# Performance work log

Measured on AMD Instinct MI355X. Metric: run time of the kernel, lower is better.

## Reference

```python
import jax, jax.numpy as jnp
import numpy as np

N_NODES, N_EDGES, D_IN, D_OUT = 50000, 800000, 64, 64
N_REL, N_TIME = 500, 1000


def setup_inputs() -> dict:
    key = jax.random.key(0)
    ks = jax.random.split(key, 14)
    xavier = lambda k, shape: jax.random.normal(k, shape, jnp.float32) * np.sqrt(2.0 / (shape[0] + shape[1])) * np.sqrt(2.0)
    return {
        "x": jax.random.normal(ks[0], (N_NODES, D_IN), jnp.float32),
        "rel_repr": jax.random.normal(ks[1], (N_REL, D_IN), jnp.float32),
        "time_emds": jax.random.normal(ks[2], (N_TIME, D_IN), jnp.float32),
        "src": jax.random.randint(ks[3], (N_EDGES,), 0, N_NODES),
        "dst": jax.random.randint(ks[4], (N_EDGES,), 0, N_NODES),
        "etype": jax.random.randint(ks[5], (N_EDGES,), 0, N_REL),
        "etime": jax.random.randint(ks[6], (N_EDGES,), 0, N_TIME),
        "trans_w": xavier(ks[7], (D_IN, D_OUT)),
        "loop_w": xavier(ks[8], (D_IN, D_OUT)),
        "w_rel": xavier(ks[9], (D_IN, D_OUT)),
        "attn_h": xavier(ks[10], (D_IN, 1)),
        "attn_t": xavier(ks[11], (D_IN, 1)),
        "attn_r": xavier(ks[12], (D_IN, 1)),
        "attn_ts": xavier(ks[13], (D_IN, 1)),
    }


def reference(x, rel_repr, time_emds, src, dst, etype, etime,
              trans_w, loop_w, w_rel, attn_h, attn_t, attn_r, attn_ts):
    n = x.shape[0]
    # per-node / per-rel / per-time scalar attention projections
    h_att = (x @ attn_h)[:, 0]          # [N]
    t_att = (x @ attn_t)[:, 0]          # [N]
    r_att = (rel_repr @ attn_r)[:, 0]   # [R]
    ts_att = (time_emds @ attn_ts)[:, 0]  # [T]
    # edge attention logits + edge_softmax grouped by destination node
    e = jax.nn.leaky_relu(h_att[src] - t_att[dst] + r_att[etype] + ts_att[etime], 0.1)  # [E]
    m = jax.ops.segment_max(e, dst, num_segments=n)
    ex = jnp.exp(e - m[dst])
    den = jax.ops.segment_sum(ex, dst, num_segments=n)
    att = (ex / den[dst])[:, None]      # [E,1]
    # message: (head + time) * (rel + time) -> trans_w -> weighted scatter-sum to dst
    time_emd = time_emds[etime]         # [E,D]
    edge_data = (x[src] + time_emd) * (rel_repr[etype] + time_emd)
    msg = (edge_data @ trans_w) * att   # [E,D_out]
    h = jax.ops.segment_sum(msg, dst, num_segments=n)
    x_out = h + x @ loop_w
    rel_out = rel_repr @ w_rel
    return (x_out, rel_out)
```

## Files before the change

kernel.cpp:

```cpp
#include <hip/hip_runtime.h>
#include <hip/hip_bf16.h>

#define N_NODES 50000
#define N_EDGES 800000
#define D 64
#define N_REL 500
#define N_TIME 1000
#define SLOTS 64
#define NODE_BLOCKS ((N_NODES + 63) / 64)
#define REL_BLOCKS  ((N_REL + 63) / 64)

#define CB 64
#define NCB ((N_NODES + CB - 1) / CB)
#define FR 64
#define NFB ((N_NODES + FR - 1) / FR)
#define SCAP 2048
#define BINCAP 8
#define BTILE 4096
#define LSLOT 48

__device__ __forceinline__ float bf2f(unsigned short u) {
    union { unsigned int i; float f; } v;
    v.i = ((unsigned int)u) << 16;
    return v.f;
}

__global__ void proj_kernel(const float* __restrict__ x,
                            const float* __restrict__ rel,
                            const float* __restrict__ tim,
                            const float* __restrict__ ah,
                            const float* __restrict__ at,
                            const float* __restrict__ ar,
                            const float* __restrict__ ats,
                            float* __restrict__ h_att, float* __restrict__ t_att,
                            float* __restrict__ r_att, float* __restrict__ ts_att,
                            unsigned short* __restrict__ x_bf,
                            int* __restrict__ cursor) {
    int gid = blockIdx.x * blockDim.x + threadIdx.x;
    if (gid < NCB) cursor[gid] = 0;
    int wave = gid >> 6;
    int lane = threadIdx.x & 63;
    const int total = N_NODES + N_REL + N_TIME;
    if (wave >= total) return;
    if (wave < N_NODES) {
        float xv = x[wave * D + lane];
        __hip_bfloat16 b = __float2bfloat16(xv);
        x_bf[wave * D + lane] = *(unsigned short*)&b;
        float s1 = xv * ah[lane];
        float s2 = xv * at[lane];
        for (int off = 32; off; off >>= 1) {
            s1 += __shfl_down(s1, off);
            s2 += __shfl_down(s2, off);
        }
        if (lane == 0) { h_att[wave] = s1; t_att[wave] = s2; }
    } else if (wave < N_NODES + N_REL) {
        int r = wave - N_NODES;
        float v = rel[r * D + lane] * ar[lane];
        for (int off = 32; off; off >>= 1) v += __shfl_down(v, off);
        if (lane == 0) r_att[r] = v;
    } else {
        int t = wave - N_NODES - N_REL;
        float v = tim[t * D + lane] * ats[lane];
        for (int off = 32; off; off >>= 1) v += __shfl_down(v, off);
        if (lane == 0) ts_att[t] = v;
    }
}

__global__ __launch_bounds__(512)
void bin_kernel(const int* __restrict__ src, const int* __restrict__ dst,
                const int* __restrict__ etype, const int* __restrict__ etime,
                const float* __restrict__ h_att, const float* __restrict__ t_att,
                const float* __restrict__ r_att, const float* __restrict__ ts_att,
                int* __restrict__ cursor, int4* __restrict__ stage) {
    __shared__ int4 bins[NCB][BINCAP];
    __shared__ int bcnt[NCB];
    int t = threadIdx.x;
    for (int k = t; k < NCB; k += 512) bcnt[k] = 0;
    __syncthreads();

    int e0 = blockIdx.x * BTILE;
    for (int j = 0; j < 8; j++) {
        int e = e0 + j * 512 + t;
        if (e < N_EDGES) {
            int s = src[e], d = dst[e], r = etype[e], tt = etime[e];
            float lg = h_att[s] - t_att[d] + r_att[r] + ts_att[tt];
            float lr = lg > 0.f ? lg : 0.1f * lg;
            float ex = __expf(lr);
            unsigned exb = __float_as_uint(ex);
            int4 rec;
            rec.x = (int)((exb & ~7u) | (unsigned)(s & 7));
            rec.y = (int)(((unsigned)(s >> 3) << 19) | ((unsigned)r << 10) | (unsigned)tt);
            rec.z = d;
            rec.w = 0;
            int k = d >> 6;
            int pos = atomicAdd(&bcnt[k], 1);
            if (pos < BINCAP) {
                bins[k][pos] = rec;
            } else {
                int g = atomicAdd(&cursor[k], 1);
                if (g < SCAP) stage[(size_t)k * SCAP + g] = rec;
            }
        }
    }
    __syncthreads();
    for (int k = t; k < NCB; k += 512) {
        int c = bcnt[k];
        if (c > BINCAP) c = BINCAP;
        if (c > 0) {
            int base = atomicAdd(&cursor[k], c);
            for (int i = 0; i < c; i++) {
                int g = base + i;
                if (g < SCAP) stage[(size_t)k * SCAP + g] = bins[k][i];
            }
        }
    }
}

__global__ __launch_bounds__(512)
void node_fused_kernel(const unsigned short* __restrict__ x_bf,
                       const float* __restrict__ rel,
                       const float* __restrict__ tim,
                       const int* __restrict__ cursor,
                       const int4* __restrict__ stage,
                       float* __restrict__ agg) {
    __shared__ int2 lslot[FR * LSLOT];
    __shared__ int lcnt[FR];
    int tid = threadIdx.x;
    int base = blockIdx.x * FR;
    int pb = blockIdx.x;

    for (int i = tid; i < FR; i += 512) lcnt[i] = 0;
    __syncthreads();

    int n = cursor[pb];
    if (n > SCAP) n = SCAP;
    for (int i = tid; i < n; i += 512) {
        int4 rec = stage[(size_t)pb * SCAP + i];
        int ln = rec.z - base;
        if ((unsigned)ln < FR) {
            int pos = atomicAdd(&lcnt[ln], 1);
            if (pos < LSLOT) lslot[ln * LSLOT + pos] = make_int2(rec.x, rec.y);
        }
    }
    __syncthreads();

    int lane = tid & 63;
    int wv = tid >> 6;
    int qw = lane >> 4;
    int ql = lane & 15;

    for (int ln = wv; ln < FR; ln += 8) {
        int d = base + ln;
        if (d >= N_NODES) break;
        int deg = lcnt[ln];
        if (deg > LSLOT) deg = LSLOT;

        int s_l = 0, r_l = 0, t_l = 0;
        float ex = 0.f;
        if (lane < deg) {
            int2 pl = lslot[ln * LSLOT + lane];
            unsigned px = (unsigned)pl.x;
            unsigned py = (unsigned)pl.y;
            ex = __uint_as_float(px & ~7u);
            s_l = (int)(((py >> 19) << 3) | (px & 7u));
            r_l = (int)((py >> 10) & 511u);
            t_l = (int)(py & 1023u);
        }
        float den = ex;
        for (int off = 32; off; off >>= 1) den += __shfl_xor(den, off);
        float att_l = (lane < deg) ? ex / den : 0.f;

        float4 acc = make_float4(0.f, 0.f, 0.f, 0.f);
        for (int i = 0; i < deg; i += 8) {
            int eiA = i + qw;
            int eiB = i + 4 + qw;
            int sA = __shfl(s_l, eiA), rA = __shfl(r_l, eiA), tA = __shfl(t_l, eiA);
            float attA = __shfl(att_l, eiA);
            int sB = __shfl(s_l, eiB), rB = __shfl(r_l, eiB), tB = __shfl(t_l, eiB);
            float attB = __shfl(att_l, eiB);
            float4  teA = *(const float4*)(tim + tA * D + ql * 4);
            ushort4 xbA = *(const ushort4*)(x_bf + sA * D + ql * 4);
            float4  rlA = *(const float4*)(rel + rA * D + ql * 4);
            float4  teB = *(const float4*)(tim + tB * D + ql * 4);
            ushort4 xbB = *(const ushort4*)(x_bf + sB * D + ql * 4);
            float4  rlB = *(const float4*)(rel + rB * D + ql * 4);
            acc.x += attA * (bf2f(xbA.x) + teA.x) * (rlA.x + teA.x);
            acc.y += attA * (bf2f(xbA.y) + teA.y) * (rlA.y + teA.y);
            acc.z += attA * (bf2f(xbA.z) + teA.z) * (rlA.z + teA.z);
            acc.w += attA * (bf2f(xbA.w) + teA.w) * (rlA.w + teA.w);
            acc.x += attB * (bf2f(xbB.x) + teB.x) * (rlB.x + teB.x);
            acc.y += attB * (bf2f(xbB.y) + teB.y) * (rlB.y + teB.y);
            acc.z += attB * (bf2f(xbB.z) + teB.z) * (rlB.z + teB.z);
            acc.w += attB * (bf2f(xbB.w) + teB.w) * (rlB.w + teB.w);
        }
        for (int off = 16; off <= 32; off <<= 1) {
            acc.x += __shfl_xor(acc.x, off);
            acc.y += __shfl_xor(acc.y, off);
            acc.z += __shfl_xor(acc.z, off);
            acc.w += __shfl_xor(acc.w, off);
        }
        if (qw == 0)
            *(float4*)(agg + (size_t)d * D + ql * 4) = acc;
    }
}

__global__ void build_kernel(const int* __restrict__ src, const int* __restrict__ dst,
                             const int* __restrict__ etype, const int* __restrict__ etime,
                             const float* __restrict__ h_att, const float* __restrict__ t_att,
                             const float* __restrict__ r_att, const float* __restrict__ ts_att,
                             int* __restrict__ cnt, int2* __restrict__ payload) {
    int e = blockIdx.x * blockDim.x + threadIdx.x;
    if (e >= N_EDGES) return;
    int s = src[e], d = dst[e], r = etype[e], t = etime[e];
    float lg = h_att[s] - t_att[d] + r_att[r] + ts_att[t];
    float lr = lg > 0.f ? lg : 0.1f * lg;
    float ex = __expf(lr);
    unsigned exb = __float_as_uint(ex);
    int2 pl;
    pl.x = (int)((exb & ~7u) | (unsigned)(s & 7));
    pl.y = (int)(((unsigned)(s >> 3) << 19) | ((unsigned)r << 10) | (unsigned)t);
    int pos = atomicAdd(&cnt[d], 1);
    if (pos < SLOTS) payload[(d << 6) + pos] = pl;
}

__global__ void node_gather_kernel(const unsigned short* __restrict__ x_bf,
                                   const float* __restrict__ rel,
                                   const float* __restrict__ tim,
                                   const int* __restrict__ cnt,
                                   const int2* __restrict__ payload,
                                   float* __restrict__ agg) {
    int d = (blockIdx.x * blockDim.x + threadIdx.x) >> 6;
    int lane = threadIdx.x & 63;
    if (d >= N_NODES) return;
    int deg = cnt[d];
    if (deg > SLOTS) deg = SLOTS;
    int s_l = 0, r_l = 0, t_l = 0;
    float ex = 0.f;
    if (lane < deg) {
        int2 pl = payload[(d << 6) + lane];
        unsigned px = (unsigned)pl.x;
        unsigned py = (unsigned)pl.y;
        ex = __uint_as_float(px & ~7u);
        s_l = (int)(((py >> 19) << 3) | (px & 7u));
        r_l = (int)((py >> 10) & 511u);
        t_l = (int)(py & 1023u);
    }
    float den = ex;
    for (int off = 32; off; off >>= 1) den += __shfl_xor(den, off);
    float att_l = (lane < deg) ? ex / den : 0.f;
    int qw = lane >> 4;
    int ql = lane & 15;
    float4 acc = make_float4(0.f, 0.f, 0.f, 0.f);
    for (int i = 0; i < deg; i += 4) {
        int ei = i + qw;
        int s = __shfl(s_l, ei);
        int r = __shfl(r_l, ei);
        int t = __shfl(t_l, ei);
        float att = __shfl(att_l, ei);
        float4  te = *(const float4*)(tim + t * D + ql * 4);
        ushort4 xb = *(const ushort4*)(x_bf + s * D + ql * 4);
        float4  rl = *(const float4*)(rel + r * D + ql * 4);
        acc.x += att * (bf2f(xb.x) + te.x) * (rl.x + te.x);
        acc.y += att * (bf2f(xb.y) + te.y) * (rl.y + te.y);
        acc.z += att * (bf2f(xb.z) + te.z) * (rl.z + te.z);
        acc.w += att * (bf2f(xb.w) + te.w) * (rl.w + te.w);
    }
    for (int off = 16; off <= 32; off <<= 1) {
        acc.x += __shfl_xor(acc.x, off);
        acc.y += __shfl_xor(acc.y, off);
        acc.z += __shfl_xor(acc.z, off);
        acc.w += __shfl_xor(acc.w, off);
    }
    if (qw == 0)
        *(float4*)(agg + (d << 7) + ql * 4) = acc;
}

__global__ __launch_bounds__(256, 2)
void out_gemm_kernel(const float* __restrict__ agg,
                     const float* __restrict__ x,
                     const float* __restrict__ rel,
                     const float* __restrict__ trans_w,
                     const float* __restrict__ loop_w,
                     const float* __restrict__ w_rel,
                     float* __restrict__ out, int astride) {
    __shared__ float Wa[D * D];
    __shared__ float Wb[D * D];
    __shared__ float At[64 * D];
    __shared__ float Xt[64 * D];
    int t = threadIdx.x;
    bool nodeb = blockIdx.x < NODE_BLOCKS;
    int row0 = nodeb ? blockIdx.x * 64 : (blockIdx.x - NODE_BLOCKS) * 64;

    for (int j = 0; j < 4; j++) {
        int idx = (t + 256 * j) * 4;
        if (nodeb) {
            *(float4*)(Wa + idx) = *(const float4*)(trans_w + idx);
            *(float4*)(Wb + idx) = *(const float4*)(loop_w + idx);
        } else {
            *(float4*)(Wa + idx) = *(const float4*)(w_rel + idx);
        }
    }
    for (int j = 0; j < 4; j++) {
        int lin = t + 256 * j;
        int rr = lin >> 4;
        int k4 = (lin & 15) << 2;
        if (nodeb) {
            int gr = row0 + rr; if (gr >= N_NODES) gr = N_NODES - 1;
            *(float4*)(At + rr * D + k4) = *(const float4*)(agg + (size_t)gr * astride + k4);
            *(float4*)(Xt + rr * D + k4) = *(const float4*)(x + (size_t)gr * D + k4);
        } else {
            int gr = row0 + rr; if (gr >= N_REL) gr = N_REL - 1;
            *(float4*)(At + rr * D + k4) = *(const float4*)(rel + (size_t)gr * D + k4);
        }
    }
    __syncthreads();

    int lane = t & 63;
    int wv = t >> 6;
    int c4 = (lane & 15) << 2;
    int r0 = wv * 16 + (lane >> 4) * 4;

    float acc[4][4];
    for (int i = 0; i < 4; i++)
        for (int c = 0; c < 4; c++) acc[i][c] = 0.f;

    if (nodeb) {
        for (int k = 0; k < D; k += 4) {
            float wt[4][4], wl[4][4];
            for (int kk = 0; kk < 4; kk++) {
                *(float4*)&wt[kk][0] = *(const float4*)(Wa + (k + kk) * D + c4);
                *(float4*)&wl[kk][0] = *(const float4*)(Wb + (k + kk) * D + c4);
            }
            for (int i = 0; i < 4; i++) {
                float a[4], xv[4];
                *(float4*)&a[0]  = *(const float4*)(At + (r0 + i) * D + k);
                *(float4*)&xv[0] = *(const float4*)(Xt + (r0 + i) * D + k);
                for (int c = 0; c < 4; c++) {
                    float s = acc[i][c];
                    for (int kk = 0; kk < 4; kk++)
                        s += a[kk] * wt[kk][c] + xv[kk] * wl[kk][c];
                    acc[i][c] = s;
                }
            }
        }
        for (int i = 0; i < 4; i++) {
            int gr = row0 + r0 + i;
            if (gr < N_NODES)
                *(float4*)(out + (size_t)gr * D + c4) = *(float4*)&acc[i][0];
        }
    } else {
        for (int k = 0; k < D; k += 4) {
            float wt[4][4];
            for (int kk = 0; kk < 4; kk++)
                *(float4*)&wt[kk][0] = *(const float4*)(Wa + (k + kk) * D + c4);
            for (int i = 0; i < 4; i++) {
                float a[4];
                *(float4*)&a[0] = *(const float4*)(At + (r0 + i) * D + k);
                for (int c = 0; c < 4; c++) {
                    float s = acc[i][c];
                    for (int kk = 0; kk < 4; kk++)
                        s += a[kk] * wt[kk][c];
                    acc[i][c] = s;
                }
            }
        }
        for (int i = 0; i < 4; i++) {
            int gr = row0 + r0 + i;
            if (gr < N_REL)
                *(float4*)(out + (size_t)(N_NODES + gr) * D + c4) = *(float4*)&acc[i][0];
        }
    }
}

extern "C" void kernel_launch(void* const* d_in, const int* in_sizes, int n_in,
                              void* d_out, int out_size, void* d_ws, size_t ws_size,
                              hipStream_t stream) {
    const float* x    = (const float*)d_in[0];
    const float* rel  = (const float*)d_in[1];
    const float* tim  = (const float*)d_in[2];
    const int* src   = (const int*)d_in[3];
    const int* dst   = (const int*)d_in[4];
    const int* etype = (const int*)d_in[5];
    const int* etime = (const int*)d_in[6];
    const float* trans_w = (const float*)d_in[7];
    const float* loop_w  = (const float*)d_in[8];
    const float* w_rel   = (const float*)d_in[9];
    const float* ah  = (const float*)d_in[10];
    const float* at  = (const float*)d_in[11];
    const float* ar  = (const float*)d_in[12];
    const float* ats = (const float*)d_in[13];

    char* ws = (char*)d_ws;
    int*   cursor         = (int*)  (ws);
    int*   cnt            = (int*)  (ws);
    float* h_att          = (float*)(ws + 200064);
    float* t_att          = (float*)(ws + 400064);
    float* r_att          = (float*)(ws + 600064);
    float* ts_att         = (float*)(ws + 602064);
    float* agg            = (float*)(ws + 1000000);
    int2*  payload        = (int2*) (ws + 1000000);
    unsigned short* x_bf  = (unsigned short*)(ws + 26600000);
    int4*  stage          = (int4*) (ws + 33000000);

    float* out = (float*)d_out;

    const size_t need = 33000000ull + (size_t)NCB * SCAP * sizeof(int4);
    const bool fused = (ws_size >= need);

    if (!fused)
        hipMemsetAsync(cnt, 0, 200000, stream);

    {
        int waves = N_NODES + N_REL + N_TIME;
        proj_kernel<<<(waves + 3) / 4, 256, 0, stream>>>(
            x, rel, tim, ah, at, ar, ats,
            h_att, t_att, r_att, ts_att, x_bf, cursor);
    }
    if (fused) {
        bin_kernel<<<(N_EDGES + BTILE - 1) / BTILE, 512, 0, stream>>>(
            src, dst, etype, etime, h_att, t_att, r_att, ts_att,
            cursor, stage);
        node_fused_kernel<<<NFB, 512, 0, stream>>>(
            x_bf, rel, tim, cursor, stage, agg);
        out_gemm_kernel<<<NODE_BLOCKS + REL_BLOCKS, 256, 0, stream>>>(
            agg, x, rel, trans_w, loop_w, w_rel, out, 64);
    } else {
        build_kernel<<<(N_EDGES + 255) / 256, 256, 0, stream>>>(
            src, dst, etype, etime, h_att, t_att, r_att, ts_att, cnt, payload);
        node_gather_kernel<<<(N_NODES + 3) / 4, 256, 0, stream>>>(
            x_bf, rel, tim, cnt, payload, agg);
        out_gemm_kernel<<<NODE_BLOCKS + REL_BLOCKS, 256, 0, stream>>>(
            agg, x, rel, trans_w, loop_w, w_rel, out, 128);
    }
}
```

Before: 192.7 us.

## Process edges flat per block with shared-memory atomic accumulation instead of per-node waves

Replaces the per-destination-node wave loop, which bucketed edges into fixed local slots and reduced with shuffles, with a flat edge-parallel loop. Each 16-thread group handles one edge record and atomically adds its weighted message into a shared-memory accumulator row, and the softmax denominator is also built with shared atomics. The aim is to remove load imbalance from varying node degrees and the per-node degree cap, at the cost of many shared-memory float atomics and contention on rows of high-degree nodes.

```diff
diff --git a/kernel.cpp b/kernel.cpp
--- a/kernel.cpp
+++ b/kernel.cpp
@@ -17,7 +17,6 @@
 #define SCAP 2048
 #define BINCAP 8
 #define BTILE 4096
-#define LSLOT 48
 
 __device__ __forceinline__ float bf2f(unsigned short u) {
     union { unsigned int i; float f; } v;
@@ -123,84 +122,85 @@
                        const int* __restrict__ cursor,
                        const int4* __restrict__ stage,
                        float* __restrict__ agg) {
-    __shared__ int2 lslot[FR * LSLOT];
-    __shared__ int lcnt[FR];
+    __shared__ int4  recs[SCAP];
+    __shared__ float acc_l[FR][65];
+    __shared__ float den[FR];
     int tid = threadIdx.x;
     int base = blockIdx.x * FR;
     int pb = blockIdx.x;
 
-    for (int i = tid; i < FR; i += 512) lcnt[i] = 0;
+    for (int i = tid; i < FR; i += 512) den[i] = 0.f;
+    for (int i = tid; i < FR * 65; i += 512) ((float*)acc_l)[i] = 0.f;
     __syncthreads();
 
     int n = cursor[pb];
     if (n > SCAP) n = SCAP;
+
     for (int i = tid; i < n; i += 512) {
         int4 rec = stage[(size_t)pb * SCAP + i];
+        recs[i] = rec;
         int ln = rec.z - base;
         if ((unsigned)ln < FR) {
-            int pos = atomicAdd(&lcnt[ln], 1);
-            if (pos < LSLOT) lslot[ln * LSLOT + pos] = make_int2(rec.x, rec.y);
-        }
-    }
-    __syncthreads();
-
-    int lane = tid & 63;
-    int wv = tid >> 6;
-    int qw = lane >> 4;
-    int ql = lane & 15;
-
-    for (int ln = wv; ln < FR; ln += 8) {
+            float ex = __uint_as_float((unsigned)rec.x & ~7u);
+            atomicAdd(&den[ln], ex);
+        }
+    }
+    __syncthreads();
+
+    int qid = tid >> 4;
+    int ql4 = (tid & 15) << 2;
+
+#define P2LOAD(REC, LN, ATT, TE, XB, RL)                                    \
+    {                                                                        \
+        unsigned px = (unsigned)(REC).x, py = (unsigned)(REC).y;             \
+        LN = ((REC).z - base) & 63;                                          \
+        ATT = __uint_as_float(px & ~7u) / den[LN];                           \
+        int s_ = (int)(((py >> 19) << 3) | (px & 7u));                       \
+        int r_ = (int)((py >> 10) & 511u);                                   \
+        int t_ = (int)(py & 1023u);                                          \
+        TE = *(const float4*)(tim + t_ * D + ql4);                           \
+        XB = *(const ushort4*)(x_bf + s_ * D + ql4);                         \
+        RL = *(const float4*)(rel + r_ * D + ql4);                           \
+    }
+#define P2ACC(LN, ATT, TE, XB, RL)                                           \
+    {                                                                        \
+        float* row_ = &acc_l[LN][ql4];                                       \
+        atomicAdd(row_ + 0, ATT * (bf2f((XB).x) + (TE).x) * ((RL).x + (TE).x)); \
+        atomicAdd(row_ + 1, ATT * (bf2f((XB).y) + (TE).y) * ((RL).y + (TE).y)); \
+        atomicAdd(row_ + 2, ATT * (bf2f((XB).z) + (TE).z) * ((RL).z + (TE).z)); \
+        atomicAdd(row_ + 3, ATT * (bf2f((XB).w) + (TE).w) * ((RL).w + (TE).w)); \
+    }
+
+    int i = qid;
+    for (; i + 32 < n; i += 64) {
+        int4 ra = recs[i];
+        int4 rb = recs[i + 32];
+        int lna, lnb; float atta, attb;
+        float4 tea, teb, rla, rlb; ushort4 xba, xbb;
+        P2LOAD(ra, lna, atta, tea, xba, rla);
+        P2LOAD(rb, lnb, attb, teb, xbb, rlb);
+        P2ACC(lna, atta, tea, xba, rla);
+        P2ACC(lnb, attb, teb, xbb, rlb);
+    }
+    if (i < n) {
+        int4 ra = recs[i];
+        int lna; float atta; float4 tea, rla; ushort4 xba;
+        P2LOAD(ra, lna, atta, tea, xba, rla);
+        P2ACC(lna, atta, tea, xba, rla);
+    }
+#undef P2LOAD
+#undef P2ACC
+    __syncthreads();
+
+    for (int j = tid; j < FR * 16; j += 512) {
+        int ln = j >> 4;
+        int c4 = (j & 15) << 2;
         int d = base + ln;
-        if (d >= N_NODES) break;
-        int deg = lcnt[ln];
-        if (deg > LSLOT) deg = LSLOT;
-
-        int s_l = 0, r_l = 0, t_l = 0;
-        float ex = 0.f;
-        if (lane < deg) {
-            int2 pl = lslot[ln * LSLOT + lane];
-            unsigned px = (unsigned)pl.x;
-            unsigned py = (unsigned)pl.y;
-            ex = __uint_as_float(px & ~7u);
-            s_l = (int)(((py >> 19) << 3) | (px & 7u));
-            r_l = (int)((py >> 10) & 511u);
-            t_l = (int)(py & 1023u);
-        }
-        float den = ex;
-        for (int off = 32; off; off >>= 1) den += __shfl_xor(den, off);
-        float att_l = (lane < deg) ? ex / den : 0.f;
-
-        float4 acc = make_float4(0.f, 0.f, 0.f, 0.f);
-        for (int i = 0; i < deg; i += 8) {
-            int eiA = i + qw;
-            int eiB = i + 4 + qw;
-            int sA = __shfl(s_l, eiA), rA = __shfl(r_l, eiA), tA = __shfl(t_l, eiA);
-            float attA = __shfl(att_l, eiA);
-            int sB = __shfl(s_l, eiB), rB = __shfl(r_l, eiB), tB = __shfl(t_l, eiB);
-            float attB = __shfl(att_l, eiB);
-            float4  teA = *(const float4*)(tim + tA * D + ql * 4);
-            ushort4 xbA = *(const ushort4*)(x_bf + sA * D + ql * 4);
-            float4  rlA = *(const float4*)(rel + rA * D + ql * 4);
-            float4  teB = *(const float4*)(tim + tB * D + ql * 4);
-            ushort4 xbB = *(const ushort4*)(x_bf + sB * D + ql * 4);
-            float4  rlB = *(const float4*)(rel + rB * D + ql * 4);
-            acc.x += attA * (bf2f(xbA.x) + teA.x) * (rlA.x + teA.x);
-            acc.y += attA * (bf2f(xbA.y) + teA.y) * (rlA.y + teA.y);
-            acc.z += attA * (bf2f(xbA.z) + teA.z) * (rlA.z + teA.z);
-            acc.w += attA * (bf2f(xbA.w) + teA.w) * (rlA.w + teA.w);
-            acc.x += attB * (bf2f(xbB.x) + teB.x) * (rlB.x + teB.x);
-            acc.y += attB * (bf2f(xbB.y) + teB.y) * (rlB.y + teB.y);
-            acc.z += attB * (bf2f(xbB.z) + teB.z) * (rlB.z + teB.z);
-            acc.w += attB * (bf2f(xbB.w) + teB.w) * (rlB.w + teB.w);
-        }
-        for (int off = 16; off <= 32; off <<= 1) {
-            acc.x += __shfl_xor(acc.x, off);
-            acc.y += __shfl_xor(acc.y, off);
-            acc.z += __shfl_xor(acc.z, off);
-            acc.w += __shfl_xor(acc.w, off);
-        }
-        if (qw == 0)
-            *(float4*)(agg + (size_t)d * D + ql * 4) = acc;
+        if (d < N_NODES) {
+            float4 v = make_float4(acc_l[ln][c4], acc_l[ln][c4 + 1],
+                                   acc_l[ln][c4 + 2], acc_l[ln][c4 + 3]);
+            *(float4*)(agg + (size_t)d * D + c4) = v;
+        }
     }
 }
 
```

New measurement: 500.8 us. +159.8%, slower.

## Fuse output GEMM into node gather kernel, split relation GEMM out

Applied to the files above, without the earlier changes.

The node aggregation kernel now keeps its aggregated rows in shared memory and multiplies them by trans_w, adding x times loop_w, inside the same block. This removes the global agg round trip and one kernel launch. Relation outputs get their own small GEMM kernel. Shared memory use rises to about 56KB per block, which may lower occupancy, and the per-node accumulators held in registers raise register pressure.

```diff
diff --git a/kernel.cpp b/kernel.cpp
--- a/kernel.cpp
+++ b/kernel.cpp
@@ -120,16 +120,37 @@
 void node_fused_kernel(const unsigned short* __restrict__ x_bf,
                        const float* __restrict__ rel,
                        const float* __restrict__ tim,
+                       const float* __restrict__ x,
+                       const float* __restrict__ trans_w,
+                       const float* __restrict__ loop_w,
                        const int* __restrict__ cursor,
                        const int4* __restrict__ stage,
-                       float* __restrict__ agg) {
-    __shared__ int2 lslot[FR * LSLOT];
-    __shared__ int lcnt[FR];
+                       float* __restrict__ out) {
+    __shared__ char  uni[FR * LSLOT * 8];
+    __shared__ int   lcnt[FR];
+    __shared__ float Wt[D * D];
+    __shared__ float Wl[D * D];
+    __shared__ float Xt[FR * D];
+    int2*  lslot = (int2*)uni;
+    float* At    = (float*)uni;
+
     int tid = threadIdx.x;
     int base = blockIdx.x * FR;
     int pb = blockIdx.x;
 
     for (int i = tid; i < FR; i += 512) lcnt[i] = 0;
+    for (int j = 0; j < 2; j++) {
+        int idx = (tid + 512 * j) * 4;
+        *(float4*)(Wt + idx) = *(const float4*)(trans_w + idx);
+        *(float4*)(Wl + idx) = *(const float4*)(loop_w + idx);
+    }
+    for (int j = 0; j < 2; j++) {
+        int lin = tid + 512 * j;
+        int rr = lin >> 4;
+        int k4 = (lin & 15) << 2;
+        int gr = base + rr; if (gr >= N_NODES) gr = N_NODES - 1;
+        *(float4*)(Xt + rr * D + k4) = *(const float4*)(x + (size_t)gr * D + k4);
+    }
     __syncthreads();
 
     int n = cursor[pb];
@@ -148,10 +169,11 @@
     int wv = tid >> 6;
     int qw = lane >> 4;
     int ql = lane & 15;
-
-    for (int ln = wv; ln < FR; ln += 8) {
-        int d = base + ln;
-        if (d >= N_NODES) break;
+    float4 acc4[8];
+
+#pragma unroll
+    for (int j = 0; j < 8; j++) {
+        int ln = wv + j * 8;
         int deg = lcnt[ln];
         if (deg > LSLOT) deg = LSLOT;
 
@@ -199,8 +221,100 @@
             acc.z += __shfl_xor(acc.z, off);
             acc.w += __shfl_xor(acc.w, off);
         }
-        if (qw == 0)
-            *(float4*)(agg + (size_t)d * D + ql * 4) = acc;
+        acc4[j] = acc;
+    }
+    __syncthreads();
+
+#pragma unroll
+    for (int j = 0; j < 8; j++) {
+        if (qw == 0) {
+            int ln = wv + j * 8;
+            *(float4*)(At + ln * D + ql * 4) = acc4[j];
+        }
+    }
+    __syncthreads();
+
+    int c4 = ql << 2;
+    int r0 = wv * 8 + qw * 2;
+    float acc[2][4];
+    for (int i = 0; i < 2; i++)
+        for (int c = 0; c < 4; c++) acc[i][c] = 0.f;
+
+    for (int k = 0; k < D; k += 4) {
+        float wt[4][4], wl[4][4];
+        for (int kk = 0; kk < 4; kk++) {
+            *(float4*)&wt[kk][0] = *(const float4*)(Wt + (k + kk) * D + c4);
+            *(float4*)&wl[kk][0] = *(const float4*)(Wl + (k + kk) * D + c4);
+        }
+        for (int i = 0; i < 2; i++) {
+            float a[4], xv[4];
+            *(float4*)&a[0]  = *(const float4*)(At + (r0 + i) * D + k);
+            *(float4*)&xv[0] = *(const float4*)(Xt + (r0 + i) * D + k);
+            for (int c = 0; c < 4; c++) {
+                float s = acc[i][c];
+                for (int kk = 0; kk < 4; kk++)
+                    s += a[kk] * wt[kk][c] + xv[kk] * wl[kk][c];
+                acc[i][c] = s;
+            }
+        }
+    }
+    for (int i = 0; i < 2; i++) {
+        int gr = base + r0 + i;
+        if (gr < N_NODES)
+            *(float4*)(out + (size_t)gr * D + c4) = *(float4*)&acc[i][0];
+    }
+}
+
+__global__ __launch_bounds__(256)
+void rel_gemm_kernel(const float* __restrict__ rel,
+                     const float* __restrict__ w_rel,
+                     float* __restrict__ out) {
+    __shared__ float Wa[D * D];
+    __shared__ float At[64 * D];
+    int t = threadIdx.x;
+    int row0 = blockIdx.x * 64;
+
+    for (int j = 0; j < 4; j++) {
+        int idx = (t + 256 * j) * 4;
+        *(float4*)(Wa + idx) = *(const float4*)(w_rel + idx);
+    }
+    for (int j = 0; j < 4; j++) {
+        int lin = t + 256 * j;
+        int rr = lin >> 4;
+        int k4 = (lin & 15) << 2;
+        int gr = row0 + rr; if (gr >= N_REL) gr = N_REL - 1;
+        *(float4*)(At + rr * D + k4) = *(const float4*)(rel + (size_t)gr * D + k4);
+    }
+    __syncthreads();
+
+    int lane = t & 63;
+    int wv = t >> 6;
+    int c4 = (lane & 15) << 2;
+    int r0 = wv * 16 + (lane >> 4) * 4;
+
+    float acc[4][4];
+    for (int i = 0; i < 4; i++)
+        for (int c = 0; c < 4; c++) acc[i][c] = 0.f;
+
+    for (int k = 0; k < D; k += 4) {
+        float wt[4][4];
+        for (int kk = 0; kk < 4; kk++)
+            *(float4*)&wt[kk][0] = *(const float4*)(Wa + (k + kk) * D + c4);
+        for (int i = 0; i < 4; i++) {
+            float a[4];
+            *(float4*)&a[0] = *(const float4*)(At + (r0 + i) * D + k);
+            for (int c = 0; c < 4; c++) {
+                float s = acc[i][c];
+                for (int kk = 0; kk < 4; kk++)
+                    s += a[kk] * wt[kk][c];
+                acc[i][c] = s;
+            }
+        }
+    }
+    for (int i = 0; i < 4; i++) {
+        int gr = row0 + r0 + i;
+        if (gr < N_REL)
+            *(float4*)(out + (size_t)(N_NODES + gr) * D + c4) = *(float4*)&acc[i][0];
     }
 }
 
@@ -421,9 +535,8 @@
             src, dst, etype, etime, h_att, t_att, r_att, ts_att,
             cursor, stage);
         node_fused_kernel<<<NFB, 512, 0, stream>>>(
-            x_bf, rel, tim, cursor, stage, agg);
-        out_gemm_kernel<<<NODE_BLOCKS + REL_BLOCKS, 256, 0, stream>>>(
-            agg, x, rel, trans_w, loop_w, w_rel, out, 64);
+            x_bf, rel, tim, x, trans_w, loop_w, cursor, stage, out);
+        rel_gemm_kernel<<<REL_BLOCKS, 256, 0, stream>>>(rel, w_rel, out);
     } else {
         build_kernel<<<(N_EDGES + 255) / 256, 256, 0, stream>>>(
             src, dst, etype, etime, h_att, t_att, r_att, ts_att, cnt, payload);
```

Result: faster. 187.3 us (-2.8%).
